# Optimization experiments

Hardware: AMD Instinct MI355X
Metric: run time of the kernel (lower is better)

## Reference

```python
import jax, jax.numpy as jnp
import numpy as np

# dims
N = 10000      # nodes
E = 320000     # edges (avg degree 32)
NS = 64        # hidden 0e scalar channels
NV = 64        # hidden 1o vector channels
EMB = 32       # node-attr embedding dim
NTYPES = 20    # max_atom_types
NB = 8         # number_of_basis (bessel)
RH = 16        # radial_neurons
L = 2          # layers
CUT = 3.5      # max_radius
NNEIGH = 32.0  # num_neighbors normalization
H = 0.1        # residual step size


def smooth_cutoff(u):
    # e3nn example smooth_cutoff applied to x/max_radius
    v = 2.0 * (u - 1.0)
    y = 0.5 * (1.0 - jnp.cos(jnp.pi * v))
    y = jnp.where(v > 0.0, 0.0, y)
    y = jnp.where(v < -1.0, 1.0, y)
    return y


def setup_inputs() -> dict:
    key = jax.random.key(0)
    ks = jax.random.split(key, 10)
    x = jax.random.normal(ks[0], (N, 6), jnp.float32)
    batch = jnp.zeros((N,), jnp.int32)
    node_attr = jax.random.randint(ks[1], (N,), 0, NTYPES)
    edge_src = jax.random.randint(ks[2], (E,), 0, N)
    # avoid self-loops (zero edge length -> NaN in sh / bessel)
    off = jax.random.randint(ks[3], (E,), 1, N)
    edge_dst = (edge_src + off) % N
    embed_table = 0.1 * jax.random.normal(ks[4], (NTYPES, EMB), jnp.float32)
    Ku = jax.random.normal(ks[5], (2, NV), jnp.float32)          # uplift (made semi-unitary via QR)
    W_sc_s = 0.05 * jax.random.normal(ks[6], (L, NS, EMB, NS + NV), jnp.float32)  # self-connection TP: scalars
    W_sc_v = 0.05 * jax.random.normal(ks[7], (L, NV, EMB, NV), jnp.float32)       # self-connection TP: vectors
    Wr1 = 0.3 * jax.random.normal(ks[8], (L, NB, RH), jnp.float32)
    br1 = jnp.zeros((L, RH), jnp.float32)
    Wr2 = 0.3 * jax.random.normal(ks[9], (L, RH, 4 * NV), jnp.float32)
    br2 = jnp.zeros((L, 4 * NV), jnp.float32)
    return {"x": x, "batch": batch, "node_attr": node_attr, "edge_src": edge_src,
            "edge_dst": edge_dst, "embed_table": embed_table, "Ku": Ku,
            "W_sc_s": W_sc_s, "W_sc_v": W_sc_v, "Wr1": Wr1, "br1": br1,
            "Wr2": Wr2, "br2": br2}


def reference(x, batch, node_attr, edge_src, edge_dst, embed_table, Ku,
              W_sc_s, W_sc_v, Wr1, br1, Wr2, br2):
    n = x.shape[0]
    a = embed_table[node_attr]                     # [n, EMB] node-attr embedding (0e scalars)
    # make uplift semi-unitary: Q^T Q = I_2
    Q, _ = jnp.linalg.qr(Ku.T)                     # [NV, 2]
    U = Q.T                                        # uplift [2, NV]
    x_v = x.reshape(n, 2, 3)                       # 2x1o: position, velocity
    y_s = jnp.zeros((n, NS), x.dtype)              # uplift has no 1o->0e path
    y_v = jnp.einsum('ncd,ch->nhd', x_v, U)        # [n, NV, 3]
    nfreq = jnp.arange(1, NB + 1, dtype=x.dtype)
    inv_deg = 1.0 / np.sqrt(NNEIGH)
    for l in range(L):
        pos = x_v[:, 0, :]
        ev = pos[edge_src] - pos[edge_dst]                          # [E, 3]
        elen = jnp.linalg.norm(ev, axis=1)                          # [E]
        sh = jnp.sqrt(3.0) * ev / elen[:, None]                     # 1x1o SH, component norm
        # bessel radial basis, scaled by sqrt(NB)
        bess = (jnp.sqrt(2.0 / CUT) * jnp.sin(jnp.pi * nfreq * elen[:, None] / CUT)
                / elen[:, None]) * np.sqrt(NB)                      # [E, NB]
        ea = smooth_cutoff(elen / CUT)[:, None] * sh                # edge_attr [E, 3]
        # radial MLP -> per-edge tensor-product weights (4 paths x NV channels)
        w = jax.nn.silu(bess @ Wr1[l] + br1[l]) @ Wr2[l] + br2[l]   # [E, 4*NV]
        wA, wB, wC, wD = jnp.split(w, 4, axis=1)
        s_src = y_s[edge_src]                                       # [E, NS]
        v_src = y_v[edge_src]                                       # [E, NV, 3]
        # TP paths: 0e x 1o -> 1o ; 1o x 1o -> 1o (cross) ; 1o x 1o -> 0e (dot, feats + gates)
        msg_v = (wA[:, :, None] * s_src[:, :, None] * ea[:, None, :]
                 + wC[:, :, None] * jnp.cross(v_src, ea[:, None, :]))  # [E, NV, 3]
        dots = jnp.einsum('evd,ed->ev', v_src, ea)                  # [E, NV]
        msg_s = jnp.concatenate([wB * dots, wD * dots], axis=1)     # [E, NS+NV]
        agg_s = jax.ops.segment_sum(msg_s, edge_dst, num_segments=n) * inv_deg
        agg_v = (jax.ops.segment_sum(msg_v.reshape(msg_v.shape[0], -1), edge_dst,
                                     num_segments=n).reshape(n, NV, 3) * inv_deg)
        # self-connection: fully-connected TP with node-attr scalars
        sc_s = jnp.einsum('ns,ne,seo->no', y_s, a, W_sc_s[l])       # [n, NS+NV]
        sc_v = jnp.einsum('nvd,ne,veu->nud', y_v, a, W_sc_v[l])     # [n, NV, 3]
        out_s = sc_s + agg_s
        out_v = sc_v + agg_v
        # gate: silu on scalar feats, sigmoid gates scale the vectors
        y_s = y_s + H * jax.nn.silu(out_s[:, :NS])
        y_v = y_v + H * jax.nn.sigmoid(out_s[:, NS:])[:, :, None] * out_v
        # project back to 2x1o
        x_v = jnp.einsum('nhd,hc->ncd', y_v, Q)
    return x_v.reshape(n, 6)
```

## Files before the change

### kernel.cpp

```cpp
#include <hip/hip_runtime.h>
#include <math.h>

#define NSC 64
#define NVC 64
#define EMB 32
#define NTYPES 20
#define NB 8
#define RH 16
#define LAYERS 2
#define CUTV 3.5f
#define HSTEP 0.1f

__device__ __forceinline__ float wave_sum(float t)
{
  #pragma unroll
  for (int mm = 1; mm < 64; mm <<= 1) t += __shfl_xor(t, mm, 64);
  return t;
}

__global__ void qr_kernel(const float* __restrict__ Ku, float* __restrict__ Q)
{
  const int i = threadIdx.x;
  float a0 = Ku[i], a1 = Ku[64 + i];
  const float xn2 = wave_sum((i >= 1) ? a0 * a0 : 0.f);
  const float alpha = __shfl(a0, 0, 64);
  const float beta0 = -copysignf(sqrtf(alpha * alpha + xn2), alpha);
  const float tau0 = (beta0 - alpha) / beta0;
  const float inv0 = 1.f / (alpha - beta0);
  const float v0 = (i == 0) ? 1.f : a0 * inv0;
  const float w = wave_sum(v0 * a1);
  a1 -= tau0 * w * v0;
  const float alpha1 = __shfl(a1, 1, 64);
  const float xn2b = wave_sum((i >= 2) ? a1 * a1 : 0.f);
  const float beta1 = -copysignf(sqrtf(alpha1 * alpha1 + xn2b), alpha1);
  const float tau1 = (beta1 - alpha1) / beta1;
  const float inv1 = 1.f / (alpha1 - beta1);
  const float v1 = (i == 0) ? 0.f : ((i == 1) ? 1.f : a1 * inv1);
  const float t1v = ((i == 1) ? 1.f : 0.f) - tau1 * v1;
  const float d = wave_sum(v0 * t1v);
  Q[i * 2 + 0] = ((i == 0) ? 1.f : 0.f) - tau0 * v0;
  Q[i * 2 + 1] = t1v - tau0 * d * v0;
}

__global__ void init_state(const float* __restrict__ x, const float* __restrict__ Qm,
                           float* __restrict__ st0, int* __restrict__ cnt, int n)
{
  const int i = blockIdx.x * 256 + threadIdx.x;
  const int node = i >> 6, lane = i & 63;
  if (node < n) {
    const float q0 = Qm[lane * 2 + 0], q1 = Qm[lane * 2 + 1];
    const float* xp = x + (size_t)node * 6;
    float* sp = st0 + (size_t)node * 256 + lane;
    sp[0]   = 0.f;
    sp[64]  = xp[0] * q0 + xp[3] * q1;
    sp[128] = xp[1] * q0 + xp[4] * q1;
    sp[192] = xp[2] * q0 + xp[5] * q1;
  }
  if (i < n) cnt[i] = 0;
}

__global__ void hist_kernel(const int* __restrict__ edst, int* __restrict__ cnt, int m)
{
  const int e = blockIdx.x * 256 + threadIdx.x;
  if (e < m) atomicAdd(&cnt[edst[e]], 1);
}

__global__ void scan_kernel(int* cnt, int* off, int n)
{
  __shared__ int lds[1024];
  const int t = threadIdx.x;
  const int CH = (n + 1023) >> 10;
  const int base = t * CH;
  int local[16];
  int run = 0;
  for (int j = 0; j < CH; ++j) {
    int v = (base + j < n) ? cnt[base + j] : 0;
    local[j] = run;
    run += v;
  }
  lds[t] = run;
  __syncthreads();
  for (int s = 1; s < 1024; s <<= 1) {
    int v = (t >= s) ? lds[t - s] : 0;
    __syncthreads();
    lds[t] += v;
    __syncthreads();
  }
  const int excl = lds[t] - run;
  for (int j = 0; j < CH; ++j) {
    if (base + j < n) {
      int o = excl + local[j];
      off[base + j] = o;
      cnt[base + j] = o;
    }
  }
  if (t == 1023) off[n] = lds[1023];
}

__global__ void scatter_kernel(const int* __restrict__ edst, int* __restrict__ cursor,
                               int* __restrict__ csr, int m)
{
  const int e = blockIdx.x * 256 + threadIdx.x;
  if (e < m) {
    int p = atomicAdd(&cursor[edst[e]], 1);
    csr[p] = e;
  }
}

__global__ void reorder_kernel(const int* __restrict__ csr,
                               const int* __restrict__ esrc, const int* __restrict__ edst,
                               int* __restrict__ esrc_s, int* __restrict__ edst_s, int m)
{
  const int k = blockIdx.x * 256 + threadIdx.x;
  if (k < m) {
    const int e = csr[k];
    esrc_s[k] = esrc[e];
    edst_s[k] = edst[e];
  }
}

__global__ void type_weights(const float* __restrict__ embed,
                             const float* __restrict__ Wss,
                             const float* __restrict__ Wsv,
                             float* __restrict__ Ws, float* __restrict__ Wv,
                             int total_s, int total_v)
{
  const int i = blockIdx.x * 256 + threadIdx.x;
  if (i < total_s) {
    const int bid = i >> 13;
    const int p = i & 8191;
    const int l = bid / NTYPES, t = bid % NTYPES;
    const int s = p >> 7, o = p & 127;
    const float* ar = embed + t * EMB;
    const float* wp = Wss + ((size_t)(l * 64 + s) * EMB) * 128 + o;
    float acc = 0.f;
    #pragma unroll
    for (int e = 0; e < EMB; ++e) acc = fmaf(ar[e], wp[e * 128], acc);
    Ws[i] = acc;
  } else {
    const int j = i - total_s;
    if (j < total_v) {
      const int bid = j >> 12;
      const int p = j & 4095;
      const int l = bid / NTYPES, t = bid % NTYPES;
      const int v = p >> 6, u = p & 63;
      const float* ar = embed + t * EMB;
      const float* wp = Wsv + ((size_t)(l * 64 + v) * EMB) * 64 + u;
      float acc = 0.f;
      #pragma unroll
      for (int e = 0; e < EMB; ++e) acc = fmaf(ar[e], wp[e * 64], acc);
      Wv[j] = acc;
    }
  }
}

__global__ void edge_geom(const float* __restrict__ xv,
                          const int* __restrict__ esrc_s, const int* __restrict__ edst_s,
                          const float* __restrict__ Wr1l, const float* __restrict__ br1l,
                          float* __restrict__ egeo, int m)
{
  const int k = blockIdx.x * 256 + threadIdx.x;
  if (k >= m) return;
  const int s = esrc_s[k], d = edst_s[k];
  const float ex = xv[(size_t)s * 6 + 0] - xv[(size_t)d * 6 + 0];
  const float ey = xv[(size_t)s * 6 + 1] - xv[(size_t)d * 6 + 1];
  const float ez = xv[(size_t)s * 6 + 2] - xv[(size_t)d * 6 + 2];
  const float len = sqrtf(ex * ex + ey * ey + ez * ez);
  const float invl = 1.f / len;
  const float u = len * (1.f / CUTV);
  const float arg = (float)M_PI * u;
  float sa, ca;
  __sincosf(arg, &sa, &ca);
  const float vv = 2.f * (u - 1.f);
  float cut = 0.5f * (1.f - (2.f * ca * ca - 1.f));
  cut = (vv > 0.f) ? 0.f : cut;
  cut = (vv < -1.f) ? 1.f : cut;
  const float cc = cut * 1.7320508075688772f * invl;
  float4* outp = (float4*)(egeo + (size_t)k * 20);
  outp[0] = make_float4(cc * ex, cc * ey, cc * ez, 0.f);
  float bess[NB];
  const float amp = 2.1380899352993948f * invl;
  const float twoc = 2.f * ca;
  float sm1 = 0.f, scur = sa;
  #pragma unroll
  for (int kk = 0; kk < NB; ++kk) {
    bess[kk] = amp * scur;
    const float snext = twoc * scur - sm1;
    sm1 = scur; scur = snext;
  }
  float hid[RH];
  #pragma unroll
  for (int j = 0; j < RH; ++j) {
    float h = br1l[j];
    #pragma unroll
    for (int kk = 0; kk < NB; ++kk) h = fmaf(bess[kk], Wr1l[kk * RH + j], h);
    hid[j] = h / (1.f + expf(-h));
  }
  outp[1] = make_float4(hid[0], hid[1], hid[2], hid[3]);
  outp[2] = make_float4(hid[4], hid[5], hid[6], hid[7]);
  outp[3] = make_float4(hid[8], hid[9], hid[10], hid[11]);
  outp[4] = make_float4(hid[12], hid[13], hid[14], hid[15]);
}

#define MLP_STEP(h, idx)                                                     \
  wA = fmaf((h), wr2A[idx], wA);                                             \
  wB = fmaf((h), wr2B[idx], wB);                                             \
  wC = fmaf((h), wr2C[idx], wC);                                             \
  wD = fmaf((h), wr2D[idx], wD);

__global__ __launch_bounds__(256, 3) void gather_update(
    const int* __restrict__ off, const int* __restrict__ esrc_s,
    const float* __restrict__ egeo,
    const float* __restrict__ st_in, const int* __restrict__ nattr,
    const float* __restrict__ Ws, const float* __restrict__ Wv,
    const float* __restrict__ Wr2l, const float* __restrict__ br2l,
    const float* __restrict__ Qm,
    float* __restrict__ st_out, float* __restrict__ xv_out, int n)
{
  const int lane = threadIdx.x & 63;
  const int node = blockIdx.x * 4 + (threadIdx.x >> 6);
  if (node >= n) return;

  float wr2A[RH], wr2B[RH], wr2C[RH], wr2D[RH];
  #pragma unroll
  for (int j = 0; j < RH; ++j) {
    const float* r = Wr2l + j * 256 + lane;
    wr2A[j] = r[0]; wr2B[j] = r[64]; wr2C[j] = r[128]; wr2D[j] = r[192];
  }
  #pragma unroll
  for (int j = 0; j < RH; ++j) {
    asm volatile("" : "+v"(wr2A[j]), "+v"(wr2B[j]), "+v"(wr2C[j]), "+v"(wr2D[j]));
  }
  const float bA = br2l[lane], bB = br2l[64 + lane],
              bC = br2l[128 + lane], bD = br2l[192 + lane];

  float aS1 = 0.f, aS2 = 0.f, aV0 = 0.f, aV1 = 0.f, aV2 = 0.f;
  const int k0 = off[node], k1 = off[node + 1];
  if (k0 < k1) {
    const int src0 = esrc_s[k0];
    const float* p0 = st_in + (size_t)src0 * 256 + lane;
    float ssN = p0[0], vxN = p0[64], vyN = p0[128], vzN = p0[192];
    const float4* g0 = (const float4*)(egeo + (size_t)k0 * 20);
    float4 N0 = g0[0], N1 = g0[1], N2 = g0[2], N3 = g0[3], N4 = g0[4];
    int srcN = (k0 + 1 < k1) ? esrc_s[k0 + 1] : src0;
    for (int k = k0; k < k1; ++k) {
      const float ss = ssN, vx = vxN, vy = vyN, vz = vzN;
      const float4 C0 = N0, C1 = N1, C2 = N2, C3 = N3, C4 = N4;
      const float* pN = st_in + (size_t)srcN * 256 + lane;
      ssN = pN[0]; vxN = pN[64]; vyN = pN[128]; vzN = pN[192];
      const int kn = (k + 1 < k1) ? (k + 1) : k;
      const float4* gp = (const float4*)(egeo + (size_t)kn * 20);
      N0 = gp[0]; N1 = gp[1]; N2 = gp[2]; N3 = gp[3]; N4 = gp[4];
      srcN = (k + 2 < k1) ? esrc_s[k + 2] : srcN;
      float wA = bA, wB = bB, wC = bC, wD = bD;
      MLP_STEP(C1.x, 0)  MLP_STEP(C1.y, 1)  MLP_STEP(C1.z, 2)  MLP_STEP(C1.w, 3)
      MLP_STEP(C2.x, 4)  MLP_STEP(C2.y, 5)  MLP_STEP(C2.z, 6)  MLP_STEP(C2.w, 7)
      MLP_STEP(C3.x, 8)  MLP_STEP(C3.y, 9)  MLP_STEP(C3.z, 10) MLP_STEP(C3.w, 11)
      MLP_STEP(C4.x, 12) MLP_STEP(C4.y, 13) MLP_STEP(C4.z, 14) MLP_STEP(C4.w, 15)
      const float dt = vx * C0.x + vy * C0.y + vz * C0.z;
      aS1 = fmaf(wB, dt, aS1);
      aS2 = fmaf(wD, dt, aS2);
      const float t = wA * ss;
      aV0 += t * C0.x + wC * (vy * C0.z - vz * C0.y);
      aV1 += t * C0.y + wC * (vz * C0.x - vx * C0.z);
      aV2 += t * C0.z + wC * (vx * C0.y - vy * C0.x);
    }
  }
  const float inv_deg = 0.17677669529663687f;

  const int ty = nattr[node];
  const float* WsT = Ws + (size_t)ty * 8192;
  const float* WvT = Wv + (size_t)ty * 4096;
  const float* own = st_in + (size_t)node * 256 + lane;
  const float ys_own = own[0], v0x = own[64], v0y = own[128], v0z = own[192];
  float oS1 = 0.f, oS2 = 0.f, oV0 = 0.f, oV1 = 0.f, oV2 = 0.f;
  #pragma unroll 4
  for (int s2 = 0; s2 < 64; ++s2) {
    const float yss = __shfl(ys_own, s2, 64);
    const float b0 = __shfl(v0x, s2, 64);
    const float b1 = __shfl(v0y, s2, 64);
    const float b2 = __shfl(v0z, s2, 64);
    const float wsA = WsT[s2 * 128 + lane];
    const float wsB = WsT[s2 * 128 + 64 + lane];
    const float wvv = WvT[s2 * 64 + lane];
    oS1 = fmaf(yss, wsA, oS1);
    oS2 = fmaf(yss, wsB, oS2);
    oV0 = fmaf(b0, wvv, oV0);
    oV1 = fmaf(b1, wvv, oV1);
    oV2 = fmaf(b2, wvv, oV2);
  }
  const float outS1 = oS1 + aS1 * inv_deg;
  const float outS2 = oS2 + aS2 * inv_deg;
  const float sig1 = 1.f / (1.f + expf(-outS1));
  const float gate = 1.f / (1.f + expf(-outS2));
  const float ysn = ys_own + HSTEP * outS1 * sig1;
  const float gf = HSTEP * gate;
  const float yvn0 = v0x + gf * (oV0 + aV0 * inv_deg);
  const float yvn1 = v0y + gf * (oV1 + aV1 * inv_deg);
  const float yvn2 = v0z + gf * (oV2 + aV2 * inv_deg);
  float* op = st_out + (size_t)node * 256 + lane;
  op[0] = ysn; op[64] = yvn0; op[128] = yvn1; op[192] = yvn2;

  const float q0 = Qm[lane * 2 + 0], q1 = Qm[lane * 2 + 1];
  float pr[6] = { yvn0 * q0, yvn1 * q0, yvn2 * q0,
                  yvn0 * q1, yvn1 * q1, yvn2 * q1 };
  #pragma unroll
  for (int mm = 1; mm < 64; mm <<= 1) {
    #pragma unroll
    for (int i = 0; i < 6; ++i) pr[i] += __shfl_xor(pr[i], mm, 64);
  }
  if (lane == 0) {
    #pragma unroll
    for (int i = 0; i < 6; ++i) xv_out[(size_t)node * 6 + i] = pr[i];
  }
}

extern "C" void kernel_launch(void* const* d_in, const int* in_sizes, int n_in,
                              void* d_out, int out_size, void* d_ws, size_t ws_size,
                              hipStream_t stream)
{
  const float* x     = (const float*)d_in[0];
  const int*   nattr = (const int*)d_in[2];
  const int*   esrc  = (const int*)d_in[3];
  const int*   edst  = (const int*)d_in[4];
  const float* embed = (const float*)d_in[5];
  const float* Ku    = (const float*)d_in[6];
  const float* Wss   = (const float*)d_in[7];
  const float* Wsv   = (const float*)d_in[8];
  const float* Wr1   = (const float*)d_in[9];
  const float* br1   = (const float*)d_in[10];
  const float* Wr2   = (const float*)d_in[11];
  const float* br2   = (const float*)d_in[12];
  const int n = in_sizes[0] / 6;
  const int m = in_sizes[3];

  char* p = (char*)d_ws;
  auto alloc = [&](size_t bytes) -> char* {
    char* r = p;
    p += (bytes + 255) & ~(size_t)255;
    return r;
  };
  int*   off    = (int*)alloc((size_t)(n + 1) * 4);
  int*   cursor = (int*)alloc((size_t)n * 4);
  int*   csr    = (int*)alloc((size_t)m * 4);
  int*   esrc_s = (int*)alloc((size_t)m * 4);
  int*   edst_s = (int*)alloc((size_t)m * 4);
  float* Q      = (float*)alloc(128 * 4);
  float* Ws     = (float*)alloc((size_t)LAYERS * NTYPES * 64 * 128 * 4);
  float* Wv     = (float*)alloc((size_t)LAYERS * NTYPES * 64 * 64 * 4);
  float* st0    = (float*)alloc((size_t)n * 256 * 4);
  float* st1    = (float*)alloc((size_t)n * 256 * 4);
  float* xvb    = (float*)alloc((size_t)n * 6 * 4);
  float* egeo   = (float*)alloc((size_t)m * 20 * 4);

  const int total_s = LAYERS * NTYPES * 64 * 128;
  const int total_v = LAYERS * NTYPES * 64 * 64;

  qr_kernel<<<1, 64, 0, stream>>>(Ku, Q);
  init_state<<<(n * 64 + 255) / 256, 256, 0, stream>>>(x, Q, st0, cursor, n);
  hist_kernel<<<(m + 255) / 256, 256, 0, stream>>>(edst, cursor, m);
  scan_kernel<<<1, 1024, 0, stream>>>(cursor, off, n);
  scatter_kernel<<<(m + 255) / 256, 256, 0, stream>>>(edst, cursor, csr, m);
  reorder_kernel<<<(m + 255) / 256, 256, 0, stream>>>(csr, esrc, edst, esrc_s, edst_s, m);
  type_weights<<<(total_s + total_v + 255) / 256, 256, 0, stream>>>(
      embed, Wss, Wsv, Ws, Wv, total_s, total_v);

  const float* xv_cur = x;
  const float* st_cur = st0;
  float* st_nxt = st1;
  for (int l = 0; l < LAYERS; ++l) {
    edge_geom<<<(m + 255) / 256, 256, 0, stream>>>(
        xv_cur, esrc_s, edst_s, Wr1 + l * NB * RH, br1 + l * RH, egeo, m);
    float* xv_out = (l == LAYERS - 1) ? (float*)d_out : xvb;
    gather_update<<<(n + 3) / 4, 256, 0, stream>>>(
        off, esrc_s, egeo, st_cur, nattr,
        Ws + (size_t)l * NTYPES * 8192, Wv + (size_t)l * NTYPES * 4096,
        Wr2 + l * RH * 256, br2 + l * 256, Q,
        st_nxt, xv_out, n);
    xv_cur = xv_out;
    float* ts = (float*)st_cur; st_cur = st_nxt; st_nxt = ts;
  }
}
```

Baseline: 317.9 us.

## Batch radial MLP across 32 edges and transpose weights through shared memory

The radial second-layer MLP moves out of the per-edge inner loop. Each lane now computes all 256 edge weights for one edge in a batch of 32 edges and stores them in a swizzled shared-memory tile, which the edge loop then reads per channel. The edge geometry buffer is split into a separate float4 direction array and a 16-float hidden array. The gather kernel now runs one 64-thread wave per node with 32 KB of LDS, which removes the register-resident Wr2 weights. In exchange it duplicates MLP work across the two half-waves and may cut occupancy.

After: 1.021 ms. 221% more time.

```diff
diff --git a/kernel.cpp b/kernel.cpp
--- a/kernel.cpp
+++ b/kernel.cpp
@@ -157,7 +157,7 @@
 __global__ void edge_geom(const float* __restrict__ xv,
                           const int* __restrict__ esrc_s, const int* __restrict__ edst_s,
                           const float* __restrict__ Wr1l, const float* __restrict__ br1l,
-                          float* __restrict__ egeo, int m)
+                          float4* __restrict__ ea4, float* __restrict__ hidb, int m)
 {
   const int k = blockIdx.x * 256 + threadIdx.x;
   if (k >= m) return;
@@ -176,8 +176,7 @@
   cut = (vv > 0.f) ? 0.f : cut;
   cut = (vv < -1.f) ? 1.f : cut;
   const float cc = cut * 1.7320508075688772f * invl;
-  float4* outp = (float4*)(egeo + (size_t)k * 20);
-  outp[0] = make_float4(cc * ex, cc * ey, cc * ez, 0.f);
+  ea4[k] = make_float4(cc * ex, cc * ey, cc * ez, 0.f);
   float bess[NB];
   const float amp = 2.1380899352993948f * invl;
   const float twoc = 2.f * ca;
@@ -196,74 +195,84 @@
     for (int kk = 0; kk < NB; ++kk) h = fmaf(bess[kk], Wr1l[kk * RH + j], h);
     hid[j] = h / (1.f + expf(-h));
   }
-  outp[1] = make_float4(hid[0], hid[1], hid[2], hid[3]);
-  outp[2] = make_float4(hid[4], hid[5], hid[6], hid[7]);
-  outp[3] = make_float4(hid[8], hid[9], hid[10], hid[11]);
-  outp[4] = make_float4(hid[12], hid[13], hid[14], hid[15]);
-}
-
-#define MLP_STEP(h, idx)                                                     \
-  wA = fmaf((h), wr2A[idx], wA);                                             \
-  wB = fmaf((h), wr2B[idx], wB);                                             \
-  wC = fmaf((h), wr2C[idx], wC);                                             \
-  wD = fmaf((h), wr2D[idx], wD);
-
-__global__ __launch_bounds__(256, 3) void gather_update(
+  float4* hp = (float4*)(hidb + (size_t)k * 16);
+  hp[0] = make_float4(hid[0],  hid[1],  hid[2],  hid[3]);
+  hp[1] = make_float4(hid[4],  hid[5],  hid[6],  hid[7]);
+  hp[2] = make_float4(hid[8],  hid[9],  hid[10], hid[11]);
+  hp[3] = make_float4(hid[12], hid[13], hid[14], hid[15]);
+}
+
+__global__ __launch_bounds__(64) void gather_update(
     const int* __restrict__ off, const int* __restrict__ esrc_s,
-    const float* __restrict__ egeo,
+    const float4* __restrict__ ea4, const float* __restrict__ hidb,
     const float* __restrict__ st_in, const int* __restrict__ nattr,
     const float* __restrict__ Ws, const float* __restrict__ Wv,
     const float* __restrict__ Wr2l, const float* __restrict__ br2l,
     const float* __restrict__ Qm,
     float* __restrict__ st_out, float* __restrict__ xv_out, int n)
 {
-  const int lane = threadIdx.x & 63;
-  const int node = blockIdx.x * 4 + (threadIdx.x >> 6);
+  __shared__ float wl[8192];
+  const int lane = threadIdx.x;
+  const int node = blockIdx.x;
   if (node >= n) return;
-
-  float wr2A[RH], wr2B[RH], wr2C[RH], wr2D[RH];
-  #pragma unroll
-  for (int j = 0; j < RH; ++j) {
-    const float* r = Wr2l + j * 256 + lane;
-    wr2A[j] = r[0]; wr2B[j] = r[64]; wr2C[j] = r[128]; wr2D[j] = r[192];
-  }
-  #pragma unroll
-  for (int j = 0; j < RH; ++j) {
-    asm volatile("" : "+v"(wr2A[j]), "+v"(wr2B[j]), "+v"(wr2C[j]), "+v"(wr2D[j]));
-  }
-  const float bA = br2l[lane], bB = br2l[64 + lane],
-              bC = br2l[128 + lane], bD = br2l[192 + lane];
+  const int el = lane & 31;
+  const int sw = lane & 31;
 
   float aS1 = 0.f, aS2 = 0.f, aV0 = 0.f, aV1 = 0.f, aV2 = 0.f;
   const int k0 = off[node], k1 = off[node + 1];
   if (k0 < k1) {
-    const int src0 = esrc_s[k0];
-    const float* p0 = st_in + (size_t)src0 * 256 + lane;
-    float ssN = p0[0], vxN = p0[64], vyN = p0[128], vzN = p0[192];
-    const float4* g0 = (const float4*)(egeo + (size_t)k0 * 20);
-    float4 N0 = g0[0], N1 = g0[1], N2 = g0[2], N3 = g0[3], N4 = g0[4];
-    int srcN = (k0 + 1 < k1) ? esrc_s[k0 + 1] : src0;
-    for (int k = k0; k < k1; ++k) {
-      const float ss = ssN, vx = vxN, vy = vyN, vz = vzN;
-      const float4 C0 = N0, C1 = N1, C2 = N2, C3 = N3, C4 = N4;
-      const float* pN = st_in + (size_t)srcN * 256 + lane;
-      ssN = pN[0]; vxN = pN[64]; vyN = pN[128]; vzN = pN[192];
-      const int kn = (k + 1 < k1) ? (k + 1) : k;
-      const float4* gp = (const float4*)(egeo + (size_t)kn * 20);
-      N0 = gp[0]; N1 = gp[1]; N2 = gp[2]; N3 = gp[3]; N4 = gp[4];
-      srcN = (k + 2 < k1) ? esrc_s[k + 2] : srcN;
-      float wA = bA, wB = bB, wC = bC, wD = bD;
-      MLP_STEP(C1.x, 0)  MLP_STEP(C1.y, 1)  MLP_STEP(C1.z, 2)  MLP_STEP(C1.w, 3)
-      MLP_STEP(C2.x, 4)  MLP_STEP(C2.y, 5)  MLP_STEP(C2.z, 6)  MLP_STEP(C2.w, 7)
-      MLP_STEP(C3.x, 8)  MLP_STEP(C3.y, 9)  MLP_STEP(C3.z, 10) MLP_STEP(C3.w, 11)
-      MLP_STEP(C4.x, 12) MLP_STEP(C4.y, 13) MLP_STEP(C4.z, 14) MLP_STEP(C4.w, 15)
-      const float dt = vx * C0.x + vy * C0.y + vz * C0.z;
-      aS1 = fmaf(wB, dt, aS1);
-      aS2 = fmaf(wD, dt, aS2);
-      const float t = wA * ss;
-      aV0 += t * C0.x + wC * (vy * C0.z - vz * C0.y);
-      aV1 += t * C0.y + wC * (vz * C0.x - vx * C0.z);
-      aV2 += t * C0.z + wC * (vx * C0.y - vy * C0.x);
+    int srcN = esrc_s[k0];
+    const float* pp = st_in + (size_t)srcN * 256 + lane;
+    float ssN = pp[0], vxN = pp[64], vyN = pp[128], vzN = pp[192];
+    float4 eaN = ea4[k0];
+    srcN = (k0 + 1 < k1) ? esrc_s[k0 + 1] : srcN;
+
+    for (int kb = k0; kb < k1; kb += 32) {
+      int ke = kb + el; if (ke > k1 - 1) ke = k1 - 1;
+      const float4* hp = (const float4*)(hidb + (size_t)ke * 16);
+      const float4 h0 = hp[0], h1 = hp[1], h2 = hp[2], h3 = hp[3];
+      const float hid[RH] = { h0.x,h0.y,h0.z,h0.w, h1.x,h1.y,h1.z,h1.w,
+                              h2.x,h2.y,h2.z,h2.w, h3.x,h3.y,h3.z,h3.w };
+      for (int ch = 0; ch < 256; ch += 4) {
+        float a0 = br2l[ch + 0];
+        float a1 = br2l[ch + 1];
+        float a2 = br2l[ch + 2];
+        float a3 = br2l[ch + 3];
+        #pragma unroll
+        for (int j = 0; j < RH; ++j) {
+          const float* wr = Wr2l + j * 256 + ch;
+          a0 = fmaf(wr[0], hid[j], a0);
+          a1 = fmaf(wr[1], hid[j], a1);
+          a2 = fmaf(wr[2], hid[j], a2);
+          a3 = fmaf(wr[3], hid[j], a3);
+        }
+        wl[(ch + 0) * 32 + (el ^ ((ch + 0) & 31))] = a0;
+        wl[(ch + 1) * 32 + (el ^ ((ch + 1) & 31))] = a1;
+        wl[(ch + 2) * 32 + (el ^ ((ch + 2) & 31))] = a2;
+        wl[(ch + 3) * 32 + (el ^ ((ch + 3) & 31))] = a3;
+      }
+      const int kend = (kb + 32 < k1) ? kb + 32 : k1;
+      for (int k = kb; k < kend; ++k) {
+        const float ss = ssN, vx = vxN, vy = vyN, vz = vzN;
+        const float4 ea = eaN;
+        const float* pN = st_in + (size_t)srcN * 256 + lane;
+        ssN = pN[0]; vxN = pN[64]; vyN = pN[128]; vzN = pN[192];
+        const int kn = (k + 1 < k1) ? k + 1 : k;
+        eaN = ea4[kn];
+        srcN = (k + 2 < k1) ? esrc_s[k + 2] : srcN;
+        const int ee = (k - kb) ^ sw;
+        const float wAv = wl[lane * 32 + ee];
+        const float wBv = wl[2048 + lane * 32 + ee];
+        const float wCv = wl[4096 + lane * 32 + ee];
+        const float wDv = wl[6144 + lane * 32 + ee];
+        const float dt = vx * ea.x + vy * ea.y + vz * ea.z;
+        aS1 = fmaf(wBv, dt, aS1);
+        aS2 = fmaf(wDv, dt, aS2);
+        const float t = wAv * ss;
+        aV0 += t * ea.x + wCv * (vy * ea.z - vz * ea.y);
+        aV1 += t * ea.y + wCv * (vz * ea.x - vx * ea.z);
+        aV2 += t * ea.z + wCv * (vx * ea.y - vy * ea.x);
+      }
     }
   }
   const float inv_deg = 0.17677669529663687f;
@@ -351,7 +360,8 @@
   float* st0    = (float*)alloc((size_t)n * 256 * 4);
   float* st1    = (float*)alloc((size_t)n * 256 * 4);
   float* xvb    = (float*)alloc((size_t)n * 6 * 4);
-  float* egeo   = (float*)alloc((size_t)m * 20 * 4);
+  float4* ea4   = (float4*)alloc((size_t)m * 16);
+  float* hidb   = (float*)alloc((size_t)m * 16 * 4);
 
   const int total_s = LAYERS * NTYPES * 64 * 128;
   const int total_v = LAYERS * NTYPES * 64 * 64;
@@ -370,10 +380,10 @@
   float* st_nxt = st1;
   for (int l = 0; l < LAYERS; ++l) {
     edge_geom<<<(m + 255) / 256, 256, 0, stream>>>(
-        xv_cur, esrc_s, edst_s, Wr1 + l * NB * RH, br1 + l * RH, egeo, m);
+        xv_cur, esrc_s, edst_s, Wr1 + l * NB * RH, br1 + l * RH, ea4, hidb, m);
     float* xv_out = (l == LAYERS - 1) ? (float*)d_out : xvb;
-    gather_update<<<(n + 3) / 4, 256, 0, stream>>>(
-        off, esrc_s, egeo, st_cur, nattr,
+    gather_update<<<n, 64, 0, stream>>>(
+        off, esrc_s, ea4, hidb, st_cur, nattr,
         Ws + (size_t)l * NTYPES * 8192, Wv + (size_t)l * NTYPES * 4096,
         Wr2 + l * RH * 256, br2 + l * 256, Q,
         st_nxt, xv_out, n);
```

## Interleave node state as float4, split edge buffers, transpose radial weights

Applied to the files above, without the earlier changes.

Node state is stored as one float4 per channel (scalar plus three vector components), so the neighbour gather in gather_update issues a single 16-byte load instead of four strided scalar loads. Edge geometry is split into a separate ea4 array and a 16-float hidden array, and Wr2 is transposed once so each lane loads its radial weights as float4 through pinned inline-asm loads. The launch bound drops from 3 to 2 waves, which gives more register headroom but may reduce occupancy for this latency-bound gather.

New measurement: 321.6 us. No clear change (+1.2%).

```diff
diff --git a/kernel.cpp b/kernel.cpp
--- a/kernel.cpp
+++ b/kernel.cpp
@@ -43,18 +43,17 @@
 }
 
 __global__ void init_state(const float* __restrict__ x, const float* __restrict__ Qm,
-                           float* __restrict__ st0, int* __restrict__ cnt, int n)
+                           float4* __restrict__ st0, int* __restrict__ cnt, int n)
 {
   const int i = blockIdx.x * 256 + threadIdx.x;
   const int node = i >> 6, lane = i & 63;
   if (node < n) {
     const float q0 = Qm[lane * 2 + 0], q1 = Qm[lane * 2 + 1];
     const float* xp = x + (size_t)node * 6;
-    float* sp = st0 + (size_t)node * 256 + lane;
-    sp[0]   = 0.f;
-    sp[64]  = xp[0] * q0 + xp[3] * q1;
-    sp[128] = xp[1] * q0 + xp[4] * q1;
-    sp[192] = xp[2] * q0 + xp[5] * q1;
+    st0[i] = make_float4(0.f,
+                         xp[0] * q0 + xp[3] * q1,
+                         xp[1] * q0 + xp[4] * q1,
+                         xp[2] * q0 + xp[5] * q1);
   }
   if (i < n) cnt[i] = 0;
 }
@@ -154,10 +153,20 @@
   }
 }
 
+__global__ void transpose_wr2(const float* __restrict__ Wr2, float* __restrict__ Wt)
+{
+  const int t = blockIdx.x * 256 + threadIdx.x;
+  if (t >= LAYERS * 256) return;
+  const int l = t >> 8, ch = t & 255;
+  #pragma unroll
+  for (int j = 0; j < RH; ++j)
+    Wt[(size_t)l * 4096 + ch * RH + j] = Wr2[(size_t)l * 4096 + j * 256 + ch];
+}
+
 __global__ void edge_geom(const float* __restrict__ xv,
                           const int* __restrict__ esrc_s, const int* __restrict__ edst_s,
                           const float* __restrict__ Wr1l, const float* __restrict__ br1l,
-                          float* __restrict__ egeo, int m)
+                          float4* __restrict__ ea4, float* __restrict__ hidb, int m)
 {
   const int k = blockIdx.x * 256 + threadIdx.x;
   if (k >= m) return;
@@ -176,8 +185,7 @@
   cut = (vv > 0.f) ? 0.f : cut;
   cut = (vv < -1.f) ? 1.f : cut;
   const float cc = cut * 1.7320508075688772f * invl;
-  float4* outp = (float4*)(egeo + (size_t)k * 20);
-  outp[0] = make_float4(cc * ex, cc * ey, cc * ez, 0.f);
+  ea4[k] = make_float4(cc * ex, cc * ey, cc * ez, 0.f);
   float bess[NB];
   const float amp = 2.1380899352993948f * invl;
   const float twoc = 2.f * ca;
@@ -196,40 +204,52 @@
     for (int kk = 0; kk < NB; ++kk) h = fmaf(bess[kk], Wr1l[kk * RH + j], h);
     hid[j] = h / (1.f + expf(-h));
   }
-  outp[1] = make_float4(hid[0], hid[1], hid[2], hid[3]);
-  outp[2] = make_float4(hid[4], hid[5], hid[6], hid[7]);
-  outp[3] = make_float4(hid[8], hid[9], hid[10], hid[11]);
-  outp[4] = make_float4(hid[12], hid[13], hid[14], hid[15]);
-}
-
-#define MLP_STEP(h, idx)                                                     \
-  wA = fmaf((h), wr2A[idx], wA);                                             \
-  wB = fmaf((h), wr2B[idx], wB);                                             \
-  wC = fmaf((h), wr2C[idx], wC);                                             \
-  wD = fmaf((h), wr2D[idx], wD);
-
-__global__ __launch_bounds__(256, 3) void gather_update(
+  float4* hp = (float4*)(hidb + (size_t)k * 16);
+  hp[0] = make_float4(hid[0],  hid[1],  hid[2],  hid[3]);
+  hp[1] = make_float4(hid[4],  hid[5],  hid[6],  hid[7]);
+  hp[2] = make_float4(hid[8],  hid[9],  hid[10], hid[11]);
+  hp[3] = make_float4(hid[12], hid[13], hid[14], hid[15]);
+}
+
+#define PIN_LOAD4(dst, addr)                                                  \
+  asm volatile("global_load_dwordx4 %0, %1, off" : "=v"(dst) : "v"(addr) : "memory")
+
+#define MLP16(res, W0, W1, W2, W3)                                            \
+  res = fmaf(g1.x, W0.x, res); res = fmaf(g1.y, W0.y, res);                   \
+  res = fmaf(g1.z, W0.z, res); res = fmaf(g1.w, W0.w, res);                   \
+  res = fmaf(g2.x, W1.x, res); res = fmaf(g2.y, W1.y, res);                   \
+  res = fmaf(g2.z, W1.z, res); res = fmaf(g2.w, W1.w, res);                   \
+  res = fmaf(g3.x, W2.x, res); res = fmaf(g3.y, W2.y, res);                   \
+  res = fmaf(g3.z, W2.z, res); res = fmaf(g3.w, W2.w, res);                   \
+  res = fmaf(g4.x, W3.x, res); res = fmaf(g4.y, W3.y, res);                   \
+  res = fmaf(g4.z, W3.z, res); res = fmaf(g4.w, W3.w, res);
+
+__global__ __launch_bounds__(256, 2) void gather_update(
     const int* __restrict__ off, const int* __restrict__ esrc_s,
-    const float* __restrict__ egeo,
-    const float* __restrict__ st_in, const int* __restrict__ nattr,
+    const float4* __restrict__ ea4, const float* __restrict__ hidb,
+    const float4* __restrict__ st_in, const int* __restrict__ nattr,
     const float* __restrict__ Ws, const float* __restrict__ Wv,
-    const float* __restrict__ Wr2l, const float* __restrict__ br2l,
+    const float* __restrict__ Wtl, const float* __restrict__ br2l,
     const float* __restrict__ Qm,
-    float* __restrict__ st_out, float* __restrict__ xv_out, int n)
+    float4* __restrict__ st_out, float* __restrict__ xv_out, int n)
 {
   const int lane = threadIdx.x & 63;
   const int node = blockIdx.x * 4 + (threadIdx.x >> 6);
   if (node >= n) return;
 
-  float wr2A[RH], wr2B[RH], wr2C[RH], wr2D[RH];
-  #pragma unroll
-  for (int j = 0; j < RH; ++j) {
-    const float* r = Wr2l + j * 256 + lane;
-    wr2A[j] = r[0]; wr2B[j] = r[64]; wr2C[j] = r[128]; wr2D[j] = r[192];
-  }
-  #pragma unroll
-  for (int j = 0; j < RH; ++j) {
-    asm volatile("" : "+v"(wr2A[j]), "+v"(wr2B[j]), "+v"(wr2C[j]), "+v"(wr2D[j]));
+  float4 WA0, WA1, WA2, WA3, WB0, WB1, WB2, WB3;
+  float4 WC0, WC1, WC2, WC3, WD0, WD1, WD2, WD3;
+  {
+    const float* pa = Wtl + (size_t)lane * RH;
+    const float* pb = Wtl + (size_t)(64 + lane) * RH;
+    const float* pc = Wtl + (size_t)(128 + lane) * RH;
+    const float* pd = Wtl + (size_t)(192 + lane) * RH;
+    PIN_LOAD4(WA0, pa);  PIN_LOAD4(WA1, pa + 4);  PIN_LOAD4(WA2, pa + 8);  PIN_LOAD4(WA3, pa + 12);
+    PIN_LOAD4(WB0, pb);  PIN_LOAD4(WB1, pb + 4);  PIN_LOAD4(WB2, pb + 8);  PIN_LOAD4(WB3, pb + 12);
+    PIN_LOAD4(WC0, pc);  PIN_LOAD4(WC1, pc + 4);  PIN_LOAD4(WC2, pc + 8);  PIN_LOAD4(WC3, pc + 12);
+    PIN_LOAD4(WD0, pd);  PIN_LOAD4(WD1, pd + 4);  PIN_LOAD4(WD2, pd + 8);  PIN_LOAD4(WD3, pd + 12);
+    asm volatile("s_waitcnt vmcnt(0)" ::: "memory");
+    __builtin_amdgcn_sched_barrier(0);
   }
   const float bA = br2l[lane], bB = br2l[64 + lane],
               bC = br2l[128 + lane], bD = br2l[192 + lane];
@@ -237,33 +257,35 @@
   float aS1 = 0.f, aS2 = 0.f, aV0 = 0.f, aV1 = 0.f, aV2 = 0.f;
   const int k0 = off[node], k1 = off[node + 1];
   if (k0 < k1) {
-    const int src0 = esrc_s[k0];
-    const float* p0 = st_in + (size_t)src0 * 256 + lane;
-    float ssN = p0[0], vxN = p0[64], vyN = p0[128], vzN = p0[192];
-    const float4* g0 = (const float4*)(egeo + (size_t)k0 * 20);
-    float4 N0 = g0[0], N1 = g0[1], N2 = g0[2], N3 = g0[3], N4 = g0[4];
-    int srcN = (k0 + 1 < k1) ? esrc_s[k0 + 1] : src0;
+    int srcN = esrc_s[k0];
+    float4 stN = st_in[(size_t)srcN * 64 + lane];
+    float4 eaN = ea4[k0];
+    const float4* hN = (const float4*)(hidb + (size_t)k0 * 16);
+    float4 g1N = hN[0], g2N = hN[1], g3N = hN[2], g4N = hN[3];
+    srcN = (k0 + 1 < k1) ? esrc_s[k0 + 1] : srcN;
+
     for (int k = k0; k < k1; ++k) {
-      const float ss = ssN, vx = vxN, vy = vyN, vz = vzN;
-      const float4 C0 = N0, C1 = N1, C2 = N2, C3 = N3, C4 = N4;
-      const float* pN = st_in + (size_t)srcN * 256 + lane;
-      ssN = pN[0]; vxN = pN[64]; vyN = pN[128]; vzN = pN[192];
+      const float4 stc = stN, ea = eaN;
+      const float4 g1 = g1N, g2 = g2N, g3 = g3N, g4 = g4N;
+      stN = st_in[(size_t)srcN * 64 + lane];
       const int kn = (k + 1 < k1) ? (k + 1) : k;
-      const float4* gp = (const float4*)(egeo + (size_t)kn * 20);
-      N0 = gp[0]; N1 = gp[1]; N2 = gp[2]; N3 = gp[3]; N4 = gp[4];
+      eaN = ea4[kn];
+      const float4* hp = (const float4*)(hidb + (size_t)kn * 16);
+      g1N = hp[0]; g2N = hp[1]; g3N = hp[2]; g4N = hp[3];
       srcN = (k + 2 < k1) ? esrc_s[k + 2] : srcN;
       float wA = bA, wB = bB, wC = bC, wD = bD;
-      MLP_STEP(C1.x, 0)  MLP_STEP(C1.y, 1)  MLP_STEP(C1.z, 2)  MLP_STEP(C1.w, 3)
-      MLP_STEP(C2.x, 4)  MLP_STEP(C2.y, 5)  MLP_STEP(C2.z, 6)  MLP_STEP(C2.w, 7)
-      MLP_STEP(C3.x, 8)  MLP_STEP(C3.y, 9)  MLP_STEP(C3.z, 10) MLP_STEP(C3.w, 11)
-      MLP_STEP(C4.x, 12) MLP_STEP(C4.y, 13) MLP_STEP(C4.z, 14) MLP_STEP(C4.w, 15)
-      const float dt = vx * C0.x + vy * C0.y + vz * C0.z;
+      MLP16(wA, WA0, WA1, WA2, WA3)
+      MLP16(wB, WB0, WB1, WB2, WB3)
+      MLP16(wC, WC0, WC1, WC2, WC3)
+      MLP16(wD, WD0, WD1, WD2, WD3)
+      const float ss = stc.x, vx = stc.y, vy = stc.z, vz = stc.w;
+      const float dt = vx * ea.x + vy * ea.y + vz * ea.z;
       aS1 = fmaf(wB, dt, aS1);
       aS2 = fmaf(wD, dt, aS2);
       const float t = wA * ss;
-      aV0 += t * C0.x + wC * (vy * C0.z - vz * C0.y);
-      aV1 += t * C0.y + wC * (vz * C0.x - vx * C0.z);
-      aV2 += t * C0.z + wC * (vx * C0.y - vy * C0.x);
+      aV0 += t * ea.x + wC * (vy * ea.z - vz * ea.y);
+      aV1 += t * ea.y + wC * (vz * ea.x - vx * ea.z);
+      aV2 += t * ea.z + wC * (vx * ea.y - vy * ea.x);
     }
   }
   const float inv_deg = 0.17677669529663687f;
@@ -271,8 +293,8 @@
   const int ty = nattr[node];
   const float* WsT = Ws + (size_t)ty * 8192;
   const float* WvT = Wv + (size_t)ty * 4096;
-  const float* own = st_in + (size_t)node * 256 + lane;
-  const float ys_own = own[0], v0x = own[64], v0y = own[128], v0z = own[192];
+  const float4 own = st_in[(size_t)node * 64 + lane];
+  const float ys_own = own.x, v0x = own.y, v0y = own.z, v0z = own.w;
   float oS1 = 0.f, oS2 = 0.f, oV0 = 0.f, oV1 = 0.f, oV2 = 0.f;
   #pragma unroll 4
   for (int s2 = 0; s2 < 64; ++s2) {
@@ -298,8 +320,7 @@
   const float yvn0 = v0x + gf * (oV0 + aV0 * inv_deg);
   const float yvn1 = v0y + gf * (oV1 + aV1 * inv_deg);
   const float yvn2 = v0z + gf * (oV2 + aV2 * inv_deg);
-  float* op = st_out + (size_t)node * 256 + lane;
-  op[0] = ysn; op[64] = yvn0; op[128] = yvn1; op[192] = yvn2;
+  st_out[(size_t)node * 64 + lane] = make_float4(ysn, yvn0, yvn1, yvn2);
 
   const float q0 = Qm[lane * 2 + 0], q1 = Qm[lane * 2 + 1];
   float pr[6] = { yvn0 * q0, yvn1 * q0, yvn2 * q0,
@@ -340,18 +361,20 @@
     p += (bytes + 255) & ~(size_t)255;
     return r;
   };
-  int*   off    = (int*)alloc((size_t)(n + 1) * 4);
-  int*   cursor = (int*)alloc((size_t)n * 4);
-  int*   csr    = (int*)alloc((size_t)m * 4);
-  int*   esrc_s = (int*)alloc((size_t)m * 4);
-  int*   edst_s = (int*)alloc((size_t)m * 4);
-  float* Q      = (float*)alloc(128 * 4);
-  float* Ws     = (float*)alloc((size_t)LAYERS * NTYPES * 64 * 128 * 4);
-  float* Wv     = (float*)alloc((size_t)LAYERS * NTYPES * 64 * 64 * 4);
-  float* st0    = (float*)alloc((size_t)n * 256 * 4);
-  float* st1    = (float*)alloc((size_t)n * 256 * 4);
-  float* xvb    = (float*)alloc((size_t)n * 6 * 4);
-  float* egeo   = (float*)alloc((size_t)m * 20 * 4);
+  int*    off    = (int*)alloc((size_t)(n + 1) * 4);
+  int*    cursor = (int*)alloc((size_t)n * 4);
+  int*    csr    = (int*)alloc((size_t)m * 4);
+  int*    esrc_s = (int*)alloc((size_t)m * 4);
+  int*    edst_s = (int*)alloc((size_t)m * 4);
+  float*  Q      = (float*)alloc(128 * 4);
+  float*  Ws     = (float*)alloc((size_t)LAYERS * NTYPES * 64 * 128 * 4);
+  float*  Wv     = (float*)alloc((size_t)LAYERS * NTYPES * 64 * 64 * 4);
+  float4* st0    = (float4*)alloc((size_t)n * 64 * 16);
+  float4* st1    = (float4*)alloc((size_t)n * 64 * 16);
+  float*  xvb    = (float*)alloc((size_t)n * 6 * 4);
+  float4* ea4    = (float4*)alloc((size_t)m * 16);
+  float*  hidb   = (float*)alloc((size_t)m * 16 * 4);
+  float*  Wt     = (float*)alloc((size_t)LAYERS * 4096 * 4);
 
   const int total_s = LAYERS * NTYPES * 64 * 128;
   const int total_v = LAYERS * NTYPES * 64 * 64;
@@ -364,20 +387,21 @@
   reorder_kernel<<<(m + 255) / 256, 256, 0, stream>>>(csr, esrc, edst, esrc_s, edst_s, m);
   type_weights<<<(total_s + total_v + 255) / 256, 256, 0, stream>>>(
       embed, Wss, Wsv, Ws, Wv, total_s, total_v);
+  transpose_wr2<<<2, 256, 0, stream>>>(Wr2, Wt);
 
   const float* xv_cur = x;
-  const float* st_cur = st0;
-  float* st_nxt = st1;
+  const float4* st_cur = st0;
+  float4* st_nxt = st1;
   for (int l = 0; l < LAYERS; ++l) {
     edge_geom<<<(m + 255) / 256, 256, 0, stream>>>(
-        xv_cur, esrc_s, edst_s, Wr1 + l * NB * RH, br1 + l * RH, egeo, m);
+        xv_cur, esrc_s, edst_s, Wr1 + l * NB * RH, br1 + l * RH, ea4, hidb, m);
     float* xv_out = (l == LAYERS - 1) ? (float*)d_out : xvb;
     gather_update<<<(n + 3) / 4, 256, 0, stream>>>(
-        off, esrc_s, egeo, st_cur, nattr,
+        off, esrc_s, ea4, hidb, st_cur, nattr,
         Ws + (size_t)l * NTYPES * 8192, Wv + (size_t)l * NTYPES * 4096,
-        Wr2 + l * RH * 256, br2 + l * 256, Q,
+        Wt + (size_t)l * 4096, br2 + l * 256, Q,
         st_nxt, xv_out, n);
     xv_cur = xv_out;
-    float* ts = (float*)st_cur; st_cur = st_nxt; st_nxt = ts;
-  }
-}
+    float4* ts = (float4*)st_cur; st_cur = st_nxt; st_nxt = ts;
+  }
+}
```
